# Kernel tuning notes

Hardware: AMD Instinct MI355X
Metric: run time of the kernel (lower is better)

The kernel has to match this reference:

```python
import jax, jax.numpy as jnp
import numpy as np

B, N, D = 16, 1024, 768
SCALE = D ** (-0.5)


def setup_inputs() -> dict:
    key = jax.random.key(0)
    ks = jax.random.split(key, 6)
    return {
        "x": jax.random.normal(ks[0], (B, N, D), dtype=jnp.float32),
        "y": jax.random.normal(ks[1], (B, N, D), dtype=jnp.float32),
        "coords": jax.random.normal(ks[2], (N, N, 6), dtype=jnp.float32),
        "W_qk": jax.random.normal(ks[3], (D, D), dtype=jnp.float32) * (D ** -0.5),
        "pos_emb": jax.random.normal(ks[4], (N, 6, 1), dtype=jnp.float32) * 0.02,
        "gating": jnp.float32(1.0),
        "temp": jnp.float32(0.1),
    }


def reference(x, y, coords, W_qk, pos_emb, gating, temp):
    # k = Linear(y), no bias; torch Linear: y @ W.T
    k = jnp.einsum('bnd,ed->bne', y, W_qk)
    # content score [B, N, N]
    patch_score = jax.nn.softmax(jnp.einsum('bnd,bmd->bnm', x, k) * SCALE, axis=-1)
    # positional score: coords [N, N, 6] @ pos_emb [N, 6, 1] -> [N, N]
    pos_score = jax.nn.softmax(jnp.einsum('pnk,pkl->pnl', coords, pos_emb)[..., 0], axis=-1)
    g = jax.nn.sigmoid(gating)
    attn = (1.0 - g) * patch_score + g * pos_score[None, :, :]  # broadcast over B
    out = jnp.einsum('bnm,bmd->bnd', attn, y)
    entropy = jnp.sum(-attn * jnp.log(attn + 1e-8), axis=-1, keepdims=True)  # [B, N, 1]
    hmap = 2.0 * (1.0 - jax.nn.sigmoid(temp * entropy))
    return out, hmap
```

## Files before the change

kernel.cpp:

```cpp
#include <hip/hip_runtime.h>
#include <hip/hip_bf16.h>
#include <cstdint>

typedef __bf16 bf16_t;
typedef __bf16 bf16x8 __attribute__((ext_vector_type(8)));
typedef __bf16 bf16x4 __attribute__((ext_vector_type(4)));
typedef float f32x4 __attribute__((ext_vector_type(4)));

static constexpr int B = 16, N = 1024, D = 768;
static constexpr float SCALE = 0.03608439182435161f;

#define ASYNC_COPY16(gptr, lptr)                                                          \
  __builtin_amdgcn_global_load_lds((const __attribute__((address_space(1))) void*)(gptr), \
                                   (__attribute__((address_space(3))) void*)(lptr), 16, 0, 0)

__device__ __forceinline__ float wave_red_max(float v) {
#pragma unroll
  for (int o = 32; o > 0; o >>= 1) v = fmaxf(v, __shfl_down(v, o, 64));
  return v;
}
__device__ __forceinline__ float wave_red_sum(float v) {
#pragma unroll
  for (int o = 32; o > 0; o >>= 1) v += __shfl_down(v, o, 64);
  return v;
}
__device__ __forceinline__ float block_max(float v, float* sm) {
  v = wave_red_max(v);
  int lane = threadIdx.x & 63, w = threadIdx.x >> 6;
  if (lane == 0) sm[w] = v;
  __syncthreads();
  return fmaxf(fmaxf(sm[0], sm[1]), fmaxf(sm[2], sm[3]));
}
__device__ __forceinline__ float block_sum(float v, float* sm) {
  v = wave_red_sum(v);
  int lane = threadIdx.x & 63, w = threadIdx.x >> 6;
  if (lane == 0) sm[w] = v;
  __syncthreads();
  return sm[0] + sm[1] + sm[2] + sm[3];
}

__global__ __launch_bounds__(256) void cast_f32_bf16_4(const float4* __restrict__ in,
                                                       bf16x4* __restrict__ out, int n4) {
  int i = blockIdx.x * 256 + threadIdx.x;
  if (i < n4) {
    float4 v = in[i];
    bf16x4 o;
    o.x = (bf16_t)v.x; o.y = (bf16_t)v.y; o.z = (bf16_t)v.z; o.w = (bf16_t)v.w;
    out[i] = o;
  }
}

__global__ __launch_bounds__(256) void cast_transpose_y(const float* __restrict__ y,
                                                        bf16_t* __restrict__ yb,
                                                        bf16_t* __restrict__ yT) {
  __shared__ bf16_t t[32][33];
  int b = blockIdx.z;
  int d0 = blockIdx.x * 32;
  int n0 = blockIdx.y * 32;
  int tx = threadIdx.x & 31;
  int ty = threadIdx.x >> 5;
  const float* src = y + (size_t)b * N * D;
  bf16_t* dstN = yb + (size_t)b * N * D;
  bf16_t* dstT = yT + (size_t)b * N * D;
#pragma unroll
  for (int r = 0; r < 4; r++) {
    int n = n0 + ty + r * 8;
    float v = src[(size_t)n * D + d0 + tx];
    bf16_t h = (bf16_t)v;
    t[ty + r * 8][tx] = h;
    dstN[(size_t)n * D + d0 + tx] = h;
  }
  __syncthreads();
#pragma unroll
  for (int r = 0; r < 4; r++) {
    int d = d0 + ty + r * 8;
    dstT[(size_t)d * N + n0 + tx] = t[tx][ty + r * 8];
  }
}

__global__ __launch_bounds__(256) void pos_softmax_k(const float* __restrict__ coords,
                                                     const float* __restrict__ pemb,
                                                     float* __restrict__ pos) {
  __shared__ float sm1[4], sm2[4];
  int p = blockIdx.x;
  int tid = threadIdx.x;
  float e[6];
#pragma unroll
  for (int k = 0; k < 6; k++) e[k] = pemb[p * 6 + k];
  float v[4];
#pragma unroll
  for (int i = 0; i < 4; i++) {
    int n = tid + i * 256;
    const float* c = coords + ((size_t)p * N + n) * 6;
    float s = 0.f;
#pragma unroll
    for (int k = 0; k < 6; k++) s += c[k] * e[k];
    v[i] = s;
  }
  float m = block_max(fmaxf(fmaxf(v[0], v[1]), fmaxf(v[2], v[3])), sm1);
  float ex[4], ls = 0.f;
#pragma unroll
  for (int i = 0; i < 4; i++) { ex[i] = __expf(v[i] - m); ls += ex[i]; }
  float sum = block_sum(ls, sm2);
  float inv = 1.f / sum;
#pragma unroll
  for (int i = 0; i < 4; i++) pos[(size_t)p * N + tid + i * 256] = ex[i] * inv;
}

__global__ __launch_bounds__(256) void attn_entropy_k(float* __restrict__ S,
                                                      const float* __restrict__ pos,
                                                      const float* __restrict__ gating,
                                                      const float* __restrict__ temp,
                                                      float* __restrict__ hmap) {
  __shared__ float sm1[4], sm2[4], sm3[4];
  size_t row = blockIdx.x;
  int q = (int)(row & (size_t)(N - 1));
  int tid = threadIdx.x;
  float* Srow = S + row * N;
  float g = 1.f / (1.f + __expf(-gating[0]));
  float s[4];
#pragma unroll
  for (int i = 0; i < 4; i++) s[i] = Srow[tid + i * 256];
  float m = block_max(fmaxf(fmaxf(s[0], s[1]), fmaxf(s[2], s[3])), sm1);
  float e[4], ls = 0.f;
#pragma unroll
  for (int i = 0; i < 4; i++) { e[i] = __expf(s[i] - m); ls += e[i]; }
  float sum = block_sum(ls, sm2);
  float inv = 1.f / sum;
  const float* prow = pos + (size_t)q * N;
  float a[4], ent = 0.f;
#pragma unroll
  for (int i = 0; i < 4; i++) {
    float patch = e[i] * inv;
    float ps = prow[tid + i * 256];
    a[i] = (1.f - g) * patch + g * ps;
    ent += -a[i] * __logf(a[i] + 1e-8f);
  }
  float E = block_sum(ent, sm3);
  __syncthreads();
  bf16_t* arow = (bf16_t*)Srow;
#pragma unroll
  for (int i = 0; i < 4; i++) arow[tid + i * 256] = (bf16_t)a[i];
  if (tid == 0) hmap[row] = 2.f / (1.f + __expf(temp[0] * E));
}

template <typename OutT, int NJ>
__global__ __launch_bounds__(512, 1) void gemm_nt_8p(const bf16_t* __restrict__ A, int lda, long long sA,
                                                     const bf16_t* __restrict__ Bm, int ldb, long long sB,
                                                     OutT* __restrict__ C, int ldc, long long sC,
                                                     int K, float scale, int swz) {
  constexpr int BN = NJ * 64;
  constexpr int BUFSZ = 32768 + NJ * 8192;
  __shared__ __align__(16) char lds_raw[2 * BUFSZ];

  const int tid = threadIdx.x;
  const int lane = tid & 63, wave = tid >> 6;
  const int wr = wave >> 2, wc = wave & 3;
  const int quad = lane >> 4, lr = lane & 15;

  int bx = blockIdx.x, by = blockIdx.y, bz = blockIdx.z;
  if (swz) {
    int Gx = gridDim.x, Gy = gridDim.y, Gz = gridDim.z;
    int i = bx + Gx * (by + Gy * bz);
    int xcd = i & 7, slot = i >> 3;
    int T = Gx * Gy;
    int bpx = Gz >> 3;
    bz = xcd * bpx + slot / T;
    int t = slot % T;
    bx = t % Gx;
    by = t / Gx;
  }
  const int tileN = bx * BN, tileM = by * 256;
  A += (long long)bz * sA + (long long)tileM * lda;
  Bm += (long long)bz * sB + (long long)tileN * ldb;
  C += (long long)bz * sC;

  const int scol = (((tid & 7) ^ ((tid >> 3) & 7)) * 8);
  const bf16_t* a_src = A + (long long)(tid >> 3) * lda + scol;
  const bf16_t* b_src = Bm + (long long)(tid >> 3) * ldb + scol;

  auto STAGE_A = [&](int t, int h) {
    char* base = lds_raw + (t & 1) * BUFSZ + h * 16384 + wave * 1024;
    const bf16_t* g = a_src + (long long)(h * 128) * lda + t * 64;
    ASYNC_COPY16(g, base);
    ASYNC_COPY16(g + (long long)64 * lda, base + 8192);
  };
  auto STAGE_B_G = [&](int t, int g) {
    char* base = lds_raw + (t & 1) * BUFSZ + 32768 + g * 8192 + wave * 1024;
    const bf16_t* gp = b_src + (long long)(g * 64) * ldb + t * 64;
    ASYNC_COPY16(gp, base);
  };
  auto WAIT_NJ = [&]() {
    if constexpr (NJ == 4) asm volatile("s_waitcnt vmcnt(4)" ::: "memory");
    else                   asm volatile("s_waitcnt vmcnt(3)" ::: "memory");
  };

  f32x4 acc[8][NJ];
#pragma unroll
  for (int i = 0; i < 8; i++)
#pragma unroll
    for (int j = 0; j < NJ; j++) acc[i][j] = (f32x4){0.f, 0.f, 0.f, 0.f};

  const int nk = K >> 6;
  const int niter = nk >> 1;

  STAGE_A(0, 0); STAGE_A(0, 1);
#pragma unroll
  for (int g = 0; g < NJ; g++) STAGE_B_G(0, g);
#pragma unroll
  for (int g = 0; g < NJ; g++) STAGE_B_G(1, g);
  WAIT_NJ();
  __builtin_amdgcn_s_barrier();

  for (int it = 0; it < niter; ++it) {
    const int t1 = 2 * it + 1;
    const bool pf = (t1 + 1) < nk;
    bf16x8 bfr[NJ][2];
#pragma unroll
    for (int q = 0; q < 8; ++q) {
      const int hb = q >> 2, qq = q & 3;
      const bf16_t* As = (const bf16_t*)(lds_raw + hb * BUFSZ + wr * 16384);
      const bf16_t* Bs = (const bf16_t*)(lds_raw + hb * BUFSZ + 32768);
      if (qq == 0) {
#pragma unroll
        for (int nj = 0; nj < NJ; ++nj)
#pragma unroll
          for (int kk = 0; kk < 2; ++kk)
            bfr[nj][kk] = *(const bf16x8*)&Bs[(wc * (NJ * 16) + nj * 16 + lr) * 64 +
                                              ((kk * 32 + quad * 8) ^ ((lr & 7) * 8))];
      }
      bf16x8 af[2][2];
#pragma unroll
      for (int s = 0; s < 2; ++s)
#pragma unroll
        for (int kk = 0; kk < 2; ++kk)
          af[s][kk] = *(const bf16x8*)&As[((qq * 2 + s) * 16 + lr) * 64 +
                                          ((kk * 32 + quad * 8) ^ ((lr & 7) * 8))];
      if (q == 0) {
        STAGE_A(t1, 0);
      } else if (q == 1) {
        STAGE_A(t1, 1);
      } else if (q == 2) {
        if (pf) { STAGE_B_G(t1 + 1, 0); STAGE_B_G(t1 + 1, 1); }
      } else if (q == 3) {
        if (pf) {
          STAGE_B_G(t1 + 1, 2);
          if constexpr (NJ == 4) STAGE_B_G(t1 + 1, 3);
          WAIT_NJ();
        } else {
          asm volatile("s_waitcnt vmcnt(0)" ::: "memory");
        }
      } else if (q == 4) {
        if (pf) STAGE_A(t1 + 1, 0);
      } else if (q == 5) {
        if (pf) STAGE_A(t1 + 1, 1);
      } else if (q == 6) {
        if (pf) { STAGE_B_G(t1 + 2, 0); STAGE_B_G(t1 + 2, 1); }
      } else {
        if (pf) {
          STAGE_B_G(t1 + 2, 2);
          if constexpr (NJ == 4) STAGE_B_G(t1 + 2, 3);
          WAIT_NJ();
        }
      }
      __builtin_amdgcn_s_barrier();
      __builtin_amdgcn_s_setprio(1);
#pragma unroll
      for (int s = 0; s < 2; ++s)
#pragma unroll
        for (int nj = 0; nj < NJ; ++nj)
#pragma unroll
          for (int kk = 0; kk < 2; ++kk)
            acc[qq * 2 + s][nj] =
                __builtin_amdgcn_mfma_f32_16x16x32_bf16(af[s][kk], bfr[nj][kk], acc[qq * 2 + s][nj], 0, 0, 0);
      __builtin_amdgcn_s_setprio(0);
      __builtin_amdgcn_s_barrier();
    }
  }
  __syncthreads();

  float* epi = (float*)lds_raw + wave * (16 * 68);
#pragma unroll
  for (int mi = 0; mi < 8; ++mi) {
#pragma unroll
    for (int nj = 0; nj < NJ; ++nj)
#pragma unroll
      for (int r = 0; r < 4; ++r)
        epi[(quad * 4 + r) * 68 + nj * 16 + lr] = acc[mi][nj][r] * scale;
    if constexpr (NJ == 4) {
      if constexpr (sizeof(OutT) == 4) {
#pragma unroll
        for (int seg = 0; seg < 4; seg++) {
          int lrow = seg * 4 + (lane >> 4);
          f32x4 v = *(const f32x4*)&epi[lrow * 68 + (lane & 15) * 4];
          long long grow = tileM + wr * 128 + mi * 16 + lrow;
          int gcol = tileN + wc * 64 + (lane & 15) * 4;
          *(f32x4*)&C[grow * ldc + gcol] = v;
        }
      } else {
#pragma unroll
        for (int seg = 0; seg < 2; seg++) {
          int lrow = seg * 8 + (lane >> 3);
          const float* p = &epi[lrow * 68 + (lane & 7) * 8];
          f32x4 v0 = *(const f32x4*)&p[0];
          f32x4 v1 = *(const f32x4*)&p[4];
          bf16x8 o;
#pragma unroll
          for (int j = 0; j < 4; j++) { o[j] = (bf16_t)v0[j]; o[j + 4] = (bf16_t)v1[j]; }
          long long grow = tileM + wr * 128 + mi * 16 + lrow;
          int gcol = tileN + wc * 64 + (lane & 7) * 8;
          *(bf16x8*)&C[grow * ldc + gcol] = o;
        }
      }
    } else {
      if constexpr (sizeof(OutT) == 4) {
#pragma unroll
        for (int seg = 0; seg < 4; seg++) {
          if (lane < 48) {
            int lrow = seg * 4 + lane / 12;
            int c4 = (lane % 12) * 4;
            f32x4 v = *(const f32x4*)&epi[lrow * 68 + c4];
            long long grow = tileM + wr * 128 + mi * 16 + lrow;
            int gcol = tileN + wc * 48 + c4;
            *(f32x4*)&C[grow * ldc + gcol] = v;
          }
        }
      } else {
#pragma unroll
        for (int seg = 0; seg < 2; seg++) {
          if (lane < 48) {
            int lrow = seg * 8 + lane / 6;
            int c8 = (lane % 6) * 8;
            const float* p = &epi[lrow * 68 + c8];
            f32x4 v0 = *(const f32x4*)&p[0];
            f32x4 v1 = *(const f32x4*)&p[4];
            bf16x8 o;
#pragma unroll
            for (int j = 0; j < 4; j++) { o[j] = (bf16_t)v0[j]; o[j + 4] = (bf16_t)v1[j]; }
            long long grow = tileM + wr * 128 + mi * 16 + lrow;
            int gcol = tileN + wc * 48 + c8;
            *(bf16x8*)&C[grow * ldc + gcol] = o;
          }
        }
      }
    }
  }
}

extern "C" void kernel_launch(void* const* d_in, const int* in_sizes, int n_in,
                              void* d_out, int out_size, void* d_ws, size_t ws_size,
                              hipStream_t stream) {
  const float* x = (const float*)d_in[0];
  const float* y = (const float*)d_in[1];
  const float* coords = (const float*)d_in[2];
  const float* W = (const float*)d_in[3];
  const float* pemb = (const float*)d_in[4];
  const float* gating = (const float*)d_in[5];
  const float* temp = (const float*)d_in[6];
  float* out = (float*)d_out;
  float* hmap = out + (size_t)B * N * D;

  char* ws = (char*)d_ws;
  bf16_t* xb = (bf16_t*)(ws + 0);
  bf16_t* yb = (bf16_t*)(ws + 25165824);
  bf16_t* yT = (bf16_t*)(ws + 50331648);
  bf16_t* Wb = (bf16_t*)(ws + 75497472);
  bf16_t* kb = (bf16_t*)(ws + 76677120);
  float* pos = (float*)(ws + 101842944);
  float* S   = (float*)(ws + 106037248);

  const int BND = B * N * D;

  cast_f32_bf16_4<<<BND / 4 / 256, 256, 0, stream>>>((const float4*)x, (bf16x4*)xb, BND / 4);
  cast_f32_bf16_4<<<(D * D / 4 + 255) / 256, 256, 0, stream>>>((const float4*)W, (bf16x4*)Wb, D * D / 4);
  cast_transpose_y<<<dim3(D / 32, N / 32, B), 256, 0, stream>>>(y, yb, yT);
  pos_softmax_k<<<N, 256, 0, stream>>>(coords, pemb, pos);

  gemm_nt_8p<bf16_t, 3><<<dim3(D / 192, (B * N) / 256, 1), 512, 0, stream>>>(
      yb, D, 0LL, Wb, D, 0LL, kb, D, 0LL, D, 1.0f, 0);

  gemm_nt_8p<float, 4><<<dim3(N / 256, N / 256, B), 512, 0, stream>>>(
      xb, D, (long long)N * D, kb, D, (long long)N * D, S, N, (long long)N * N, D, SCALE, 1);

  attn_entropy_k<<<B * N, 256, 0, stream>>>(S, pos, gating, temp, hmap);

  gemm_nt_8p<float, 3><<<dim3(D / 192, N / 256, B), 512, 0, stream>>>(
      (const bf16_t*)S, 2 * N, (long long)N * 2 * N, yT, N, (long long)N * D, out, D, (long long)N * D, N, 1.0f, 1);
}
```

Before: 289.7 us.

## Store attention scores in fp16, vectorize transpose and softmax, swizzle projection GEMM

The score GEMM now writes S as fp16 instead of fp32, which halves the S write and the read in the entropy kernel. The attention probabilities are written in place as bf16 at a dense stride, so the final GEMM reads contiguous rows. The y cast-transpose moves to 64x64 tiles with float4 loads and bf16x4 stores, and the entropy kernel uses vectorized contiguous loads. The K-projection GEMM gets an XCD-aware block swizzle. Storing scores in fp16 risks precision loss or overflow for large logits, though scaled scores here should be small.

```diff
diff --git a/kernel.cpp b/kernel.cpp
--- a/kernel.cpp
+++ b/kernel.cpp
@@ -6,6 +6,7 @@
 typedef __bf16 bf16x8 __attribute__((ext_vector_type(8)));
 typedef __bf16 bf16x4 __attribute__((ext_vector_type(4)));
 typedef float f32x4 __attribute__((ext_vector_type(4)));
+typedef _Float16 f16x4 __attribute__((ext_vector_type(4)));
 
 static constexpr int B = 16, N = 1024, D = 768;
 static constexpr float SCALE = 0.03608439182435161f;
@@ -53,28 +54,32 @@
 __global__ __launch_bounds__(256) void cast_transpose_y(const float* __restrict__ y,
                                                         bf16_t* __restrict__ yb,
                                                         bf16_t* __restrict__ yT) {
-  __shared__ bf16_t t[32][33];
+  __shared__ bf16_t t[64][68];
   int b = blockIdx.z;
-  int d0 = blockIdx.x * 32;
-  int n0 = blockIdx.y * 32;
-  int tx = threadIdx.x & 31;
-  int ty = threadIdx.x >> 5;
+  int d0 = blockIdx.x * 64;
+  int n0 = blockIdx.y * 64;
+  int tx = threadIdx.x & 15;
+  int ty = threadIdx.x >> 4;
   const float* src = y + (size_t)b * N * D;
   bf16_t* dstN = yb + (size_t)b * N * D;
   bf16_t* dstT = yT + (size_t)b * N * D;
 #pragma unroll
   for (int r = 0; r < 4; r++) {
-    int n = n0 + ty + r * 8;
-    float v = src[(size_t)n * D + d0 + tx];
-    bf16_t h = (bf16_t)v;
-    t[ty + r * 8][tx] = h;
-    dstN[(size_t)n * D + d0 + tx] = h;
+    int n = n0 + ty + r * 16;
+    float4 v = *(const float4*)&src[(size_t)n * D + d0 + tx * 4];
+    bf16x4 h;
+    h.x = (bf16_t)v.x; h.y = (bf16_t)v.y; h.z = (bf16_t)v.z; h.w = (bf16_t)v.w;
+    *(bf16x4*)&dstN[(size_t)n * D + d0 + tx * 4] = h;
+    *(bf16x4*)&t[ty + r * 16][tx * 4] = h;
   }
   __syncthreads();
 #pragma unroll
-  for (int r = 0; r < 4; r++) {
-    int d = d0 + ty + r * 8;
-    dstT[(size_t)d * N + n0 + tx] = t[tx][ty + r * 8];
+  for (int w = 0; w < 4; w++) {
+    int dd = (threadIdx.x >> 4) + w * 16;
+    int ng = (threadIdx.x & 15) * 4;
+    bf16x4 o;
+    o.x = t[ng + 0][dd]; o.y = t[ng + 1][dd]; o.z = t[ng + 2][dd]; o.w = t[ng + 3][dd];
+    *(bf16x4*)&dstT[(size_t)(d0 + dd) * N + n0 + ng] = o;
   }
 }
 
@@ -107,7 +112,7 @@
   for (int i = 0; i < 4; i++) pos[(size_t)p * N + tid + i * 256] = ex[i] * inv;
 }
 
-__global__ __launch_bounds__(256) void attn_entropy_k(float* __restrict__ S,
+__global__ __launch_bounds__(256) void attn_entropy_k(_Float16* __restrict__ S,
                                                       const float* __restrict__ pos,
                                                       const float* __restrict__ gating,
                                                       const float* __restrict__ temp,
@@ -116,31 +121,31 @@
   size_t row = blockIdx.x;
   int q = (int)(row & (size_t)(N - 1));
   int tid = threadIdx.x;
-  float* Srow = S + row * N;
+  _Float16* Srow = S + row * N;
   float g = 1.f / (1.f + __expf(-gating[0]));
+  f16x4 v = *(const f16x4*)&Srow[tid * 4];
   float s[4];
 #pragma unroll
-  for (int i = 0; i < 4; i++) s[i] = Srow[tid + i * 256];
+  for (int i = 0; i < 4; i++) s[i] = (float)v[i];
   float m = block_max(fmaxf(fmaxf(s[0], s[1]), fmaxf(s[2], s[3])), sm1);
   float e[4], ls = 0.f;
 #pragma unroll
   for (int i = 0; i < 4; i++) { e[i] = __expf(s[i] - m); ls += e[i]; }
   float sum = block_sum(ls, sm2);
   float inv = 1.f / sum;
-  const float* prow = pos + (size_t)q * N;
+  float4 ps = *(const float4*)&pos[(size_t)q * N + tid * 4];
+  float psv[4] = {ps.x, ps.y, ps.z, ps.w};
   float a[4], ent = 0.f;
 #pragma unroll
   for (int i = 0; i < 4; i++) {
     float patch = e[i] * inv;
-    float ps = prow[tid + i * 256];
-    a[i] = (1.f - g) * patch + g * ps;
+    a[i] = (1.f - g) * patch + g * psv[i];
     ent += -a[i] * __logf(a[i] + 1e-8f);
   }
   float E = block_sum(ent, sm3);
-  __syncthreads();
-  bf16_t* arow = (bf16_t*)Srow;
-#pragma unroll
-  for (int i = 0; i < 4; i++) arow[tid + i * 256] = (bf16_t)a[i];
+  bf16x4 o;
+  o.x = (bf16_t)a[0]; o.y = (bf16_t)a[1]; o.z = (bf16_t)a[2]; o.w = (bf16_t)a[3];
+  *(bf16x4*)&((bf16_t*)Srow)[tid * 4] = o;
   if (tid == 0) hmap[row] = 2.f / (1.f + __expf(temp[0] * E));
 }
 
@@ -159,7 +164,7 @@
   const int quad = lane >> 4, lr = lane & 15;
 
   int bx = blockIdx.x, by = blockIdx.y, bz = blockIdx.z;
-  if (swz) {
+  if (swz == 1) {
     int Gx = gridDim.x, Gy = gridDim.y, Gz = gridDim.z;
     int i = bx + Gx * (by + Gy * bz);
     int xcd = i & 7, slot = i >> 3;
@@ -169,6 +174,13 @@
     int t = slot % T;
     bx = t % Gx;
     by = t / Gx;
+  } else if (swz == 2) {
+    int Gx = gridDim.x, Gy = gridDim.y;
+    int i = bx + Gx * by;
+    int xcd = i & 7, slot = i >> 3;
+    int ypx = Gy >> 3;
+    by = xcd * ypx + slot / Gx;
+    bx = slot % Gx;
   }
   const int tileN = bx * BN, tileM = by * 256;
   A += (long long)bz * sA + (long long)tileM * lda;
@@ -304,12 +316,12 @@
           const float* p = &epi[lrow * 68 + (lane & 7) * 8];
           f32x4 v0 = *(const f32x4*)&p[0];
           f32x4 v1 = *(const f32x4*)&p[4];
-          bf16x8 o;
-#pragma unroll
-          for (int j = 0; j < 4; j++) { o[j] = (bf16_t)v0[j]; o[j + 4] = (bf16_t)v1[j]; }
+          __align__(16) OutT o8[8];
+#pragma unroll
+          for (int j = 0; j < 4; j++) { o8[j] = (OutT)v0[j]; o8[j + 4] = (OutT)v1[j]; }
           long long grow = tileM + wr * 128 + mi * 16 + lrow;
           int gcol = tileN + wc * 64 + (lane & 7) * 8;
-          *(bf16x8*)&C[grow * ldc + gcol] = o;
+          *(f32x4*)&C[grow * ldc + gcol] = *(const f32x4*)o8;
         }
       }
     } else {
@@ -334,12 +346,12 @@
             const float* p = &epi[lrow * 68 + c8];
             f32x4 v0 = *(const f32x4*)&p[0];
             f32x4 v1 = *(const f32x4*)&p[4];
-            bf16x8 o;
-#pragma unroll
-            for (int j = 0; j < 4; j++) { o[j] = (bf16_t)v0[j]; o[j + 4] = (bf16_t)v1[j]; }
+            __align__(16) OutT o8[8];
+#pragma unroll
+            for (int j = 0; j < 4; j++) { o8[j] = (OutT)v0[j]; o8[j + 4] = (OutT)v1[j]; }
             long long grow = tileM + wr * 128 + mi * 16 + lrow;
             int gcol = tileN + wc * 48 + c8;
-            *(bf16x8*)&C[grow * ldc + gcol] = o;
+            *(f32x4*)&C[grow * ldc + gcol] = *(const f32x4*)o8;
           }
         }
       }
@@ -367,23 +379,23 @@
   bf16_t* Wb = (bf16_t*)(ws + 75497472);
   bf16_t* kb = (bf16_t*)(ws + 76677120);
   float* pos = (float*)(ws + 101842944);
-  float* S   = (float*)(ws + 106037248);
+  _Float16* S = (_Float16*)(ws + 106037248);
 
   const int BND = B * N * D;
 
   cast_f32_bf16_4<<<BND / 4 / 256, 256, 0, stream>>>((const float4*)x, (bf16x4*)xb, BND / 4);
   cast_f32_bf16_4<<<(D * D / 4 + 255) / 256, 256, 0, stream>>>((const float4*)W, (bf16x4*)Wb, D * D / 4);
-  cast_transpose_y<<<dim3(D / 32, N / 32, B), 256, 0, stream>>>(y, yb, yT);
+  cast_transpose_y<<<dim3(D / 64, N / 64, B), 256, 0, stream>>>(y, yb, yT);
   pos_softmax_k<<<N, 256, 0, stream>>>(coords, pemb, pos);
 
   gemm_nt_8p<bf16_t, 3><<<dim3(D / 192, (B * N) / 256, 1), 512, 0, stream>>>(
-      yb, D, 0LL, Wb, D, 0LL, kb, D, 0LL, D, 1.0f, 0);
-
-  gemm_nt_8p<float, 4><<<dim3(N / 256, N / 256, B), 512, 0, stream>>>(
+      yb, D, 0LL, Wb, D, 0LL, kb, D, 0LL, D, 1.0f, 2);
+
+  gemm_nt_8p<_Float16, 4><<<dim3(N / 256, N / 256, B), 512, 0, stream>>>(
       xb, D, (long long)N * D, kb, D, (long long)N * D, S, N, (long long)N * N, D, SCALE, 1);
 
   attn_entropy_k<<<B * N, 256, 0, stream>>>(S, pos, gating, temp, hmap);
 
   gemm_nt_8p<float, 3><<<dim3(D / 192, N / 256, B), 512, 0, stream>>>(
-      (const bf16_t*)S, 2 * N, (long long)N * 2 * N, yT, N, (long long)N * D, out, D, (long long)N * D, N, 1.0f, 1);
-}
+      (const bf16_t*)S, N, (long long)N * N, yT, N, (long long)N * D, out, D, (long long)N * D, N, 1.0f, 1);
+}
```

New measurement: 286.2 us. Within noise of the previous version (-1.2%).
